# Optimization experiments

Hardware: AMD Instinct MI355X
Metric: run time of the kernel (lower is better)

Reference implementation:

```python
import jax, jax.numpy as jnp
import numpy as np
import math

DIM = 768
HEADS = 12
HEAD_DIM = DIM // HEADS
HIDDEN = DIM * 4
EPS = 1e-5

def _ln(x, g, b):
    mu = jnp.mean(x, axis=-1, keepdims=True)
    var = jnp.var(x, axis=-1, keepdims=True)
    return (x - mu) * jax.lax.rsqrt(var + EPS) * g + b

def setup_inputs() -> dict:
    key = jax.random.key(0)
    ks = jax.random.split(key, 16)
    def w(k, shape, fan_in):
        lim = 1.0 / math.sqrt(fan_in)
        return jax.random.uniform(k, shape, jnp.float32, -lim, lim)
    x = jax.random.normal(ks[0], (16, 1024, DIM), jnp.float32)
    return {
        "x": x,
        "ln1_g": jnp.ones((DIM,)), "ln1_b": jnp.zeros((DIM,)),
        "qkv_w": w(ks[1], (DIM, 3 * DIM), DIM), "qkv_b": w(ks[2], (3 * DIM,), DIM),
        "proj_w": w(ks[3], (DIM, DIM), DIM), "proj_b": w(ks[4], (DIM,), DIM),
        "ln2_g": jnp.ones((DIM,)), "ln2_b": jnp.zeros((DIM,)),
        "fc1_w": w(ks[5], (DIM, HIDDEN), DIM), "fc1_b": w(ks[6], (HIDDEN,), DIM),
        "fc2_w": w(ks[7], (HIDDEN, DIM), HIDDEN), "fc2_b": w(ks[8], (DIM,), HIDDEN),
        "ln3_g": jnp.ones((DIM,)), "ln3_b": jnp.zeros((DIM,)),
    }

def reference(x, ln1_g, ln1_b, qkv_w, qkv_b, proj_w, proj_b,
              ln2_g, ln2_b, fc1_w, fc1_b, fc2_w, fc2_b, ln3_g, ln3_b):
    B, N, _ = x.shape
    x_norm1 = _ln(x, ln1_g, ln1_b)
    qkv = x_norm1 @ qkv_w + qkv_b                      # [B,N,3*DIM]
    qkv = qkv.reshape(B, N, 3, HEADS, HEAD_DIM).transpose(2, 0, 3, 1, 4)
    q, k, v = qkv[0], qkv[1], qkv[2]                   # [B,H,N,Dh]
    scores = jnp.einsum('bhnd,bhmd->bhnm', q, k) / math.sqrt(HEAD_DIM)
    probs = jax.nn.softmax(scores, axis=-1)
    ctx = jnp.einsum('bhnm,bhmd->bhnd', probs, v)      # [B,H,N,Dh]
    ctx = ctx.transpose(0, 2, 1, 3).reshape(B, N, DIM)
    attn_out = ctx @ proj_w + proj_b
    x_after_attn = x + attn_out
    ff_in = _ln(x_after_attn, ln2_g, ln2_b)
    # NOTE: residual is taken from the NORMALIZED tensor, as in the source
    ff_hidden = jax.nn.gelu(ff_in @ fc1_w + fc1_b, approximate=False)
    ff_out = ff_hidden @ fc2_w + fc2_b
    x_after_mlp = ff_in + ff_out
    return _ln(x_after_mlp, ln3_g, ln3_b)
```

## Files before the change

kernel.cpp:

```cpp
#include <hip/hip_runtime.h>
#include <hip/hip_bf16.h>
#include <math.h>

#define NSEQ 1024
#define BB   16
#define DIM  768
#define NH   12
#define DH   64
#define HID  3072
#define QKVN 2304

typedef __hip_bfloat16 bf16;
typedef __attribute__((ext_vector_type(8))) short short8;
typedef __attribute__((ext_vector_type(4))) float floatx4;

__device__ __forceinline__ float b2f(bf16 v) { return __bfloat162float(v); }
__device__ __forceinline__ bf16 f2b(float v) { return __float2bfloat16(v); }
__device__ __forceinline__ unsigned short bbits(float v) {
    bf16 x = __float2bfloat16(v);
    return *reinterpret_cast<unsigned short*>(&x);
}
__device__ __forceinline__ float us2f(unsigned short u) {
    return b2f(*reinterpret_cast<bf16*>(&u));
}

__device__ __forceinline__ void gload16(const bf16* g, bf16* l) {
    __builtin_amdgcn_global_load_lds(
        (__attribute__((address_space(1))) void*)g,
        (__attribute__((address_space(3))) void*)l,
        16, 0, 0);
}

__device__ __forceinline__ bool mode_f32(const unsigned* sent) {
    return sent[0] == 0x3F800000u;
}
__device__ __forceinline__ float ldM(const void* p, long i, bool f32) {
    return f32 ? ((const float*)p)[i] : b2f(((const bf16*)p)[i]);
}

__global__ __launch_bounds__(256)
void ln_kernel(const void* __restrict__ in, long in_off, int in_ext,
               const void* __restrict__ g, const void* __restrict__ b,
               void* __restrict__ out, long out_off, int out_ext,
               const unsigned* __restrict__ sent) {
    bool m = mode_f32(sent);
    bool inF = in_ext && m, outF = out_ext && m;
    int wid = threadIdx.x >> 6, lane = threadIdx.x & 63;
    long row = (long)blockIdx.x * 4 + wid;
    float v[12];
    for (int j = 0; j < 3; ++j) {
        long idx = in_off + row * DIM + lane * 4 + j * 256;
        if (inF) {
            float4 t = *(const float4*)((const float*)in + idx);
            v[j * 4 + 0] = t.x; v[j * 4 + 1] = t.y;
            v[j * 4 + 2] = t.z; v[j * 4 + 3] = t.w;
        } else {
            ushort4 t = *(const ushort4*)((const bf16*)in + idx);
            v[j * 4 + 0] = us2f(t.x); v[j * 4 + 1] = us2f(t.y);
            v[j * 4 + 2] = us2f(t.z); v[j * 4 + 3] = us2f(t.w);
        }
    }
    float s = 0.f, q = 0.f;
    for (int i = 0; i < 12; ++i) { s += v[i]; q += v[i] * v[i]; }
    for (int off = 1; off < 64; off <<= 1) {
        s += __shfl_xor(s, off);
        q += __shfl_xor(q, off);
    }
    float mean = s * (1.0f / DIM);
    float var  = q * (1.0f / DIM) - mean * mean;
    float rs   = rsqrtf(var + 1e-5f);
    for (int j = 0; j < 3; ++j) {
        int col = lane * 4 + j * 256;
        float gv[4], bv[4];
        if (m) {
            float4 tg = *(const float4*)((const float*)g + col);
            float4 tb = *(const float4*)((const float*)b + col);
            gv[0] = tg.x; gv[1] = tg.y; gv[2] = tg.z; gv[3] = tg.w;
            bv[0] = tb.x; bv[1] = tb.y; bv[2] = tb.z; bv[3] = tb.w;
        } else {
            ushort4 tg = *(const ushort4*)((const bf16*)g + col);
            ushort4 tb = *(const ushort4*)((const bf16*)b + col);
            gv[0] = us2f(tg.x); gv[1] = us2f(tg.y); gv[2] = us2f(tg.z); gv[3] = us2f(tg.w);
            bv[0] = us2f(tb.x); bv[1] = us2f(tb.y); bv[2] = us2f(tb.z); bv[3] = us2f(tb.w);
        }
        float o[4];
        for (int k = 0; k < 4; ++k)
            o[k] = (v[j * 4 + k] - mean) * rs * gv[k] + bv[k];
        long idx = out_off + row * DIM + col;
        if (outF) {
            float4 t; t.x = o[0]; t.y = o[1]; t.z = o[2]; t.w = o[3];
            *(float4*)((float*)out + idx) = t;
        } else {
            ushort4 t;
            t.x = bbits(o[0]); t.y = bbits(o[1]); t.z = bbits(o[2]); t.w = bbits(o[3]);
            *(ushort4*)((bf16*)out + idx) = t;
        }
    }
}

__global__ __launch_bounds__(256)
void transpose_w(const void* __restrict__ W, bf16* __restrict__ WT,
                 int K, int N, const unsigned* __restrict__ sent) {
    bool m = mode_f32(sent);
    __shared__ float T[32][33];
    int t = threadIdx.x;
    int k0 = blockIdx.y * 32, n0 = blockIdx.x * 32;
    for (int i = 0; i < 4; ++i) {
        int r = (t >> 5) + i * 8, c = t & 31;
        T[r][c] = ldM(W, (long)(k0 + r) * N + n0 + c, m);
    }
    __syncthreads();
    for (int i = 0; i < 4; ++i) {
        int rr = (t >> 5) + i * 8, cc = t & 31;
        WT[(long)(n0 + rr) * K + k0 + cc] = f2b(T[cc][rr]);
    }
}

__global__ __launch_bounds__(256)
void v_transpose(const bf16* __restrict__ qkv, bf16* __restrict__ VT) {
    __shared__ bf16 T[32][33];
    int t = threadIdx.x;
    int c0 = blockIdx.x * 32, n0 = blockIdx.y * 32;
    const bf16* qb = qkv + (long)blockIdx.z * NSEQ * QKVN;
    bf16* vb = VT + (long)blockIdx.z * DIM * NSEQ;
    for (int i = 0; i < 4; ++i) {
        int r = (t >> 5) + i * 8, c = t & 31;
        T[r][c] = qb[(long)(n0 + r) * QKVN + 2 * DIM + c0 + c];
    }
    __syncthreads();
    for (int i = 0; i < 4; ++i) {
        int rr = (t >> 5) + i * 8, cc = t & 31;
        vb[(long)(c0 + rr) * NSEQ + n0 + cc] = T[cc][rr];
    }
}

__global__ __launch_bounds__(256)
void gemm_mfma(const bf16* __restrict__ A, const bf16* __restrict__ WT,
               const void* __restrict__ bias,
               const void* __restrict__ resid, long resid_off, int resid_ext,
               bf16* __restrict__ C, int M, int N, int K, int gelu_flag,
               const unsigned* __restrict__ sent) {
    __shared__ __align__(16) bf16 SH[2][128 * 64];
    bf16* As = SH[0];
    bf16* Bs = SH[1];
    int t = threadIdx.x;
    int wid = t >> 6, lane = t & 63;
    int quad = lane >> 4, l16 = lane & 15;
    int wm = (wid & 1) * 64, wn = (wid >> 1) * 64;
    int m0 = blockIdx.y * 128, n0 = blockIdx.x * 128;

    floatx4 acc[4][4];
    for (int i = 0; i < 4; ++i) for (int j = 0; j < 4; ++j)
        acc[i][j] = (floatx4){0.f, 0.f, 0.f, 0.f};

    int srow = lane >> 3;
    int sgc  = (lane & 7) ^ (srow & 7);

    for (int k0 = 0; k0 < K; k0 += 64) {
        #pragma unroll
        for (int j = 0; j < 4; ++j) {
            int br = (wid * 4 + j) * 8;
            gload16(&A[(long)(m0 + br + srow) * K + k0 + sgc * 8],
                    &As[br * 64]);
            gload16(&WT[(long)(n0 + br + srow) * K + k0 + sgc * 8],
                    &Bs[br * 64]);
        }
        __syncthreads();
        for (int ks = 0; ks < 2; ++ks) {
            int cq = ks * 4 + quad;
            short8 af[4], bfr[4];
            for (int mi = 0; mi < 4; ++mi)
                af[mi] = *(const short8*)(
                    &As[(wm + mi * 16 + l16) * 64 + ((cq ^ (l16 & 7)) << 3)]);
            for (int ni = 0; ni < 4; ++ni)
                bfr[ni] = *(const short8*)(
                    &Bs[(wn + ni * 16 + l16) * 64 + ((cq ^ (l16 & 7)) << 3)]);
            for (int mi = 0; mi < 4; ++mi)
                for (int ni = 0; ni < 4; ++ni)
                    acc[mi][ni] = __builtin_amdgcn_mfma_f32_16x16x32_bf16(
                        af[mi], bfr[ni], acc[mi][ni], 0, 0, 0);
        }
        __syncthreads();
    }

    bool md = mode_f32(sent);

    bf16* wreg = &SH[wid >> 1][(wid & 1) * (64 * 64)];
    for (int mi = 0; mi < 4; ++mi) {
        for (int ni = 0; ni < 4; ++ni) {
            int col = n0 + wn + ni * 16 + l16;
            float bv = ldM(bias, col, md);
            int chunk = ni * 2 + (l16 >> 3);
            int csw = chunk ^ (quad << 1);
            for (int r = 0; r < 4; ++r) {
                float v = acc[mi][ni][r] + bv;
                if (gelu_flag) v = 0.5f * v * (1.0f + erff(v * 0.70710678118f));
                int row_l = mi * 16 + quad * 4 + r;
                wreg[row_l * 64 + csw * 8 + (l16 & 7)] = f2b(v);
            }
        }
    }
    for (int s = 0; s < 8; ++s) {
        int row_l = s * 8 + (lane >> 3);
        int csw = (lane & 7) ^ (((row_l >> 2) & 3) << 1);
        short8 cv = *(const short8*)(&wreg[row_l * 64 + csw * 8]);
        long idx = (long)(m0 + wm + row_l) * N + n0 + wn + (lane & 7) * 8;
        if (resid) {
            float f[8];
            if (resid_ext && md) {
                const float* rp = (const float*)resid + resid_off + idx;
                float4 r0 = *(const float4*)(rp);
                float4 r1 = *(const float4*)(rp + 4);
                f[0] = r0.x; f[1] = r0.y; f[2] = r0.z; f[3] = r0.w;
                f[4] = r1.x; f[5] = r1.y; f[6] = r1.z; f[7] = r1.w;
            } else {
                const bf16* rp = resid_ext ? (const bf16*)resid + resid_off + idx
                                           : (const bf16*)resid + idx;
                short8 rv = *(const short8*)(rp);
                for (int j = 0; j < 8; ++j) {
                    short sj = rv[j];
                    f[j] = b2f(*reinterpret_cast<bf16*>(&sj));
                }
            }
            short8 ov;
            for (int j = 0; j < 8; ++j) {
                short sj = cv[j];
                float v = b2f(*reinterpret_cast<bf16*>(&sj)) + f[j];
                ov[j] = (short)bbits(v);
            }
            *(short8*)(&C[idx]) = ov;
        } else {
            *(short8*)(&C[idx]) = cv;
        }
    }
}

__global__ __launch_bounds__(256)
void attn_kernel(const bf16* __restrict__ qkv, const bf16* __restrict__ VT,
                 bf16* __restrict__ ctx) {
    const bf16* qb  = qkv + (long)blockIdx.z * NSEQ * QKVN;
    bf16*       cb  = ctx + (long)blockIdx.z * NSEQ * DIM;
    int h = blockIdx.y;
    const bf16* vtb = VT + ((long)blockIdx.z * DIM + h * DH) * NSEQ;
    int q0 = blockIdx.x * 64;
    int t = threadIdx.x;
    int wid = t >> 6, lane = t & 63;
    int quad = lane >> 4, l16 = lane & 15;

    __shared__ __align__(16) bf16 Qs[64 * 64];
    __shared__ __align__(16) bf16 Ks[64 * 64];
    __shared__ __align__(16) bf16 Vt[64 * 64];
    __shared__ bf16 Ps[4 * 16 * 72];

    int srow = t >> 2, cb2 = (t & 3) * 2;
    int sw0 = (cb2 ^ (srow & 7)) << 3;
    int sw1 = ((cb2 + 1) ^ (srow & 7)) << 3;

    {
        const bf16* src = qb + (long)(q0 + srow) * QKVN + h * DH + cb2 * 8;
        *(uint4*)(&Qs[srow * 64 + sw0]) = *(const uint4*)(src);
        *(uint4*)(&Qs[srow * 64 + sw1]) = *(const uint4*)(src + 8);
    }

    floatx4 Oc[4];
    for (int nt = 0; nt < 4; ++nt) Oc[nt] = (floatx4){0.f, 0.f, 0.f, 0.f};
    float mrow = -1e30f, lrow = 0.0f;

    bf16* Pw = &Ps[wid * 16 * 72];
    short8 af[2];
    bool afload = false;

    for (int kt = 0; kt < NSEQ / 64; ++kt) {
        __syncthreads();
        {
            const bf16* src = qb + (long)(kt * 64 + srow) * QKVN + DIM + h * DH + cb2 * 8;
            *(uint4*)(&Ks[srow * 64 + sw0]) = *(const uint4*)(src);
            *(uint4*)(&Ks[srow * 64 + sw1]) = *(const uint4*)(src + 8);
        }
        {
            const bf16* src = vtb + (long)srow * NSEQ + kt * 64 + cb2 * 8;
            *(uint4*)(&Vt[srow * 64 + sw0]) = *(const uint4*)(src);
            *(uint4*)(&Vt[srow * 64 + sw1]) = *(const uint4*)(src + 8);
        }
        __syncthreads();

        if (!afload) {
            for (int ks = 0; ks < 2; ++ks) {
                int cq = ks * 4 + quad;
                af[ks] = *(const short8*)(
                    &Qs[(wid * 16 + l16) * 64 + ((cq ^ (l16 & 7)) << 3)]);
            }
            afload = true;
        }

        floatx4 Sc[4];
        for (int kb = 0; kb < 4; ++kb) {
            floatx4 s = (floatx4){0.f, 0.f, 0.f, 0.f};
            for (int ks = 0; ks < 2; ++ks) {
                int cq = ks * 4 + quad;
                short8 kf = *(const short8*)(
                    &Ks[(kb * 16 + l16) * 64 + ((cq ^ (l16 & 7)) << 3)]);
                s = __builtin_amdgcn_mfma_f32_16x16x32_bf16(kf, af[ks], s, 0, 0, 0);
            }
            Sc[kb] = s;
        }

        float mx = -1e30f;
        for (int kb = 0; kb < 4; ++kb)
            for (int r = 0; r < 4; ++r)
                mx = fmaxf(mx, Sc[kb][r]);
        mx = fmaxf(mx, __shfl_xor(mx, 16));
        mx = fmaxf(mx, __shfl_xor(mx, 32));
        float smax = mx * 0.125f;
        if (!__all(smax <= mrow + 8.0f)) {
            float mnew = fmaxf(mrow, smax);
            float alpha = __expf(mrow - mnew);
            mrow = mnew;
            lrow *= alpha;
            float al[4];
            for (int r = 0; r < 4; ++r)
                al[r] = __shfl(alpha, quad * 4 + r);
            for (int nt = 0; nt < 4; ++nt)
                for (int r = 0; r < 4; ++r)
                    Oc[nt][r] *= al[r];
        }
        float su = 0.f;
        for (int kb = 0; kb < 4; ++kb)
            for (int r = 0; r < 4; ++r) {
                float p = __expf(Sc[kb][r] * 0.125f - mrow);
                Sc[kb][r] = p;
                su += p;
            }
        su += __shfl_xor(su, 16);
        su += __shfl_xor(su, 32);
        lrow += su;

        for (int kb = 0; kb < 4; ++kb)
            for (int r = 0; r < 4; ++r)
                Pw[l16 * 72 + kb * 16 + quad * 4 + r] = f2b(Sc[kb][r]);

        for (int ks = 0; ks < 2; ++ks) {
            int cq = ks * 4 + quad;
            short8 pf = *(const short8*)(&Pw[l16 * 72 + ks * 32 + quad * 8]);
            for (int nt = 0; nt < 4; ++nt) {
                short8 vf = *(const short8*)(
                    &Vt[(nt * 16 + l16) * 64 + ((cq ^ (l16 & 7)) << 3)]);
                Oc[nt] = __builtin_amdgcn_mfma_f32_16x16x32_bf16(pf, vf, Oc[nt], 0, 0, 0);
            }
        }
    }

    float inv[4];
    for (int r = 0; r < 4; ++r)
        inv[r] = 1.0f / __shfl(lrow, quad * 4 + r);
    for (int nt = 0; nt < 4; ++nt) {
        for (int r = 0; r < 4; ++r) {
            int q = q0 + wid * 16 + quad * 4 + r;
            cb[(long)q * DIM + h * DH + nt * 16 + l16] = f2b(Oc[nt][r] * inv[r]);
        }
    }
}

extern "C" void kernel_launch(void* const* d_in, const int* in_sizes, int n_in,
                              void* d_out, int out_size, void* d_ws, size_t ws_size,
                              hipStream_t stream) {
    const void* x      = d_in[0];
    const void* ln1_g  = d_in[1];
    const void* ln1_b  = d_in[2];
    const void* qkv_w  = d_in[3];
    const void* qkv_b  = d_in[4];
    const void* proj_w = d_in[5];
    const void* proj_b = d_in[6];
    const void* ln2_g  = d_in[7];
    const void* ln2_b  = d_in[8];
    const void* fc1_w  = d_in[9];
    const void* fc1_b  = d_in[10];
    const void* fc2_w  = d_in[11];
    const void* fc2_b  = d_in[12];
    const void* ln3_g  = d_in[13];
    const void* ln3_b  = d_in[14];
    const unsigned* sent = (const unsigned*)d_in[1];

    bf16* WTq = (bf16*)d_ws;
    bf16* WTp = WTq + (long)QKVN * DIM;
    bf16* WT1 = WTp + (long)DIM * DIM;
    bf16* WT2 = WT1 + (long)HID * DIM;
    bf16* A0  = WT2 + (long)DIM * HID;
    size_t wbytes = ((size_t)QKVN * DIM + (size_t)DIM * DIM +
                     (size_t)HID * DIM + (size_t)DIM * HID) * sizeof(bf16);

    int G = BB;
    while (G > 1 && wbytes + (size_t)G * NSEQ * 7680 > ws_size) G >>= 1;
    int TG = G * NSEQ;
    int CHT = (TG / 2 < 8192) ? TG / 2 : 8192;
    int nch = TG / CHT;

    bf16* W0 = A0;
    bf16* WQ = A0 + (long)TG * DIM;
    bf16* X2 = WQ;
    bf16* WH = WQ + (long)TG * DIM;
    bf16* VT = WQ + (long)TG * QKVN;

    transpose_w<<<dim3(QKVN / 32, DIM / 32), 256, 0, stream>>>(qkv_w, WTq, DIM, QKVN, sent);
    transpose_w<<<dim3(DIM / 32, DIM / 32), 256, 0, stream>>>(proj_w, WTp, DIM, DIM, sent);
    transpose_w<<<dim3(HID / 32, DIM / 32), 256, 0, stream>>>(fc1_w, WT1, DIM, HID, sent);
    transpose_w<<<dim3(DIM / 32, HID / 32), 256, 0, stream>>>(fc2_w, WT2, HID, DIM, sent);

    for (int g = 0; g < BB / G; ++g) {
        long xoff = (long)g * TG * DIM;

        ln_kernel<<<TG / 4, 256, 0, stream>>>(x, xoff, 1, ln1_g, ln1_b, W0, 0, 0, sent);
        gemm_mfma<<<dim3(QKVN / 128, TG / 128), 256, 0, stream>>>(
            W0, WTq, qkv_b, nullptr, 0, 0, WQ, TG, QKVN, DIM, 0, sent);
        v_transpose<<<dim3(DIM / 32, NSEQ / 32, G), 256, 0, stream>>>(WQ, VT);
        attn_kernel<<<dim3(NSEQ / 64, NH, G), 256, 0, stream>>>(WQ, VT, W0);
        gemm_mfma<<<dim3(DIM / 128, TG / 128), 256, 0, stream>>>(
            W0, WTp, proj_b, x, xoff, 1, X2, TG, DIM, DIM, 0, sent);
        ln_kernel<<<TG / 4, 256, 0, stream>>>(X2, 0, 0, ln2_g, ln2_b, X2, 0, 0, sent);
        for (int c = 0; c < nch; ++c) {
            bf16* ffc = X2 + (long)c * CHT * DIM;
            gemm_mfma<<<dim3(HID / 128, CHT / 128), 256, 0, stream>>>(
                ffc, WT1, fc1_b, nullptr, 0, 0, WH, CHT, HID, DIM, 1, sent);
            gemm_mfma<<<dim3(DIM / 128, CHT / 128), 256, 0, stream>>>(
                WH, WT2, fc2_b, ffc, 0, 0, W0 + (long)c * CHT * DIM,
                CHT, DIM, HID, 0, sent);
        }
        ln_kernel<<<TG / 4, 256, 0, stream>>>(W0, 0, 0, ln3_g, ln3_b, d_out, xoff, 1, sent);
    }
}
```

Before: 715.4 us.

## Add 256x256-tile 512-thread MFMA GEMM for QKV and FC1 projections

Introduces a new GEMM kernel with 256x256 output tiles, 8 waves, a 4-stage LDS ring buffer with two tiles of prefetch in flight, swizzled LDS layout, and an LDS-staged epilogue for coalesced stores. It replaces the 128x128 GEMM for the QKV and FC1 projections to raise arithmetic intensity and data reuse per block. The trade-off is more LDS and register use per block and fewer blocks in the grid, which may reduce occupancy and wave-level load balance across CUs.

```diff
diff --git a/kernel.cpp b/kernel.cpp
--- a/kernel.cpp
+++ b/kernel.cpp
@@ -235,6 +235,106 @@
     }
 }
 
+__device__ __forceinline__ void stg256(const bf16* src, long row0, int K, int k0,
+                                       bf16* lds, int wid, int lane, int sgc) {
+    gload16(&src[(row0 + wid * 16 + (lane >> 2)) * (long)K + k0 + sgc * 8],
+            &lds[wid * 16 * 32]);
+}
+
+__global__ __launch_bounds__(512)
+void gemm_mfma256(const bf16* __restrict__ A, const bf16* __restrict__ WT,
+                  const void* __restrict__ bias, bf16* __restrict__ C,
+                  int M, int N, int K, int gelu_flag,
+                  const unsigned* __restrict__ sent) {
+    __shared__ __align__(16) bf16 SH[4][2][256 * 32];
+    int t = threadIdx.x;
+    int wid = t >> 6, lane = t & 63;
+    int quad = lane >> 4, l16 = lane & 15;
+    int wm = (wid >> 2) * 128, wn = (wid & 3) * 64;
+    long m0 = (long)blockIdx.y * 256, n0 = (long)blockIdx.x * 256;
+    int sgc = (lane & 3) ^ ((lane >> 2) & 3);
+    int rsw = (quad ^ (l16 & 3)) << 3;
+
+    floatx4 acc[8][4];
+    #pragma unroll
+    for (int i = 0; i < 8; ++i)
+        #pragma unroll
+        for (int j = 0; j < 4; ++j)
+            acc[i][j] = (floatx4){0.f, 0.f, 0.f, 0.f};
+
+    int NT = K >> 5;
+    for (int tt = 0; tt < 2; ++tt) {
+        int k0 = tt * 32;
+        stg256(A,  m0,       K, k0, SH[tt][0],            wid, lane, sgc);
+        stg256(A,  m0 + 128, K, k0, SH[tt][0] + 128 * 32, wid, lane, sgc);
+        stg256(WT, n0,       K, k0, SH[tt][1],            wid, lane, sgc);
+        stg256(WT, n0 + 128, K, k0, SH[tt][1] + 128 * 32, wid, lane, sgc);
+    }
+    asm volatile("s_waitcnt vmcnt(4)" ::: "memory");
+    __builtin_amdgcn_s_barrier();
+
+    for (int kt = 0; kt < NT; ++kt) {
+        bf16* Ab = SH[kt & 3][0];
+        bf16* Bb = SH[kt & 3][1];
+        bool pre = (kt + 2 < NT);
+        int b2 = (kt + 2) & 3;
+        int k2 = (kt + 2) * 32;
+
+        short8 bfr[4];
+        #pragma unroll
+        for (int ni = 0; ni < 4; ++ni)
+            bfr[ni] = *(const short8*)(&Bb[(wn + ni * 16 + l16) * 32 + rsw]);
+
+        #pragma unroll
+        for (int p = 0; p < 4; ++p) {
+            if (pre) {
+                if (p == 0) stg256(A,  m0,       K, k2, SH[b2][0],            wid, lane, sgc);
+                if (p == 1) stg256(A,  m0 + 128, K, k2, SH[b2][0] + 128 * 32, wid, lane, sgc);
+                if (p == 2) stg256(WT, n0,       K, k2, SH[b2][1],            wid, lane, sgc);
+                if (p == 3) stg256(WT, n0 + 128, K, k2, SH[b2][1] + 128 * 32, wid, lane, sgc);
+            }
+            short8 af0 = *(const short8*)(&Ab[(wm + (p * 2)     * 16 + l16) * 32 + rsw]);
+            short8 af1 = *(const short8*)(&Ab[(wm + (p * 2 + 1) * 16 + l16) * 32 + rsw]);
+            __builtin_amdgcn_s_setprio(1);
+            #pragma unroll
+            for (int ni = 0; ni < 4; ++ni) {
+                acc[p * 2][ni] = __builtin_amdgcn_mfma_f32_16x16x32_bf16(
+                    af0, bfr[ni], acc[p * 2][ni], 0, 0, 0);
+                acc[p * 2 + 1][ni] = __builtin_amdgcn_mfma_f32_16x16x32_bf16(
+                    af1, bfr[ni], acc[p * 2 + 1][ni], 0, 0, 0);
+            }
+            __builtin_amdgcn_s_setprio(0);
+        }
+        if (pre) asm volatile("s_waitcnt vmcnt(4)" ::: "memory");
+        else     asm volatile("s_waitcnt vmcnt(0)" ::: "memory");
+        __builtin_amdgcn_s_barrier();
+    }
+
+    bool md = mode_f32(sent);
+    bf16* wreg = &SH[0][0][0] + wid * 8192;
+    for (int mi = 0; mi < 8; ++mi) {
+        for (int ni = 0; ni < 4; ++ni) {
+            long col = n0 + wn + ni * 16 + l16;
+            float bv = ldM(bias, col, md);
+            int chunk = ni * 2 + (l16 >> 3);
+            int csw = chunk ^ (quad << 1);
+            for (int r = 0; r < 4; ++r) {
+                float v = acc[mi][ni][r] + bv;
+                if (gelu_flag) v = 0.5f * v * (1.0f + erff(v * 0.70710678118f));
+                int row_l = mi * 16 + quad * 4 + r;
+                wreg[row_l * 64 + csw * 8 + (l16 & 7)] = f2b(v);
+            }
+        }
+    }
+    for (int s = 0; s < 16; ++s) {
+        int row_l = s * 8 + (lane >> 3);
+        int csw = (lane & 7) ^ (((row_l >> 2) & 3) << 1);
+        short8 cv = *(const short8*)(&wreg[row_l * 64 + csw * 8]);
+        long idx = (m0 + wm + row_l) * N + n0 + wn + (lane & 7) * 8;
+        *(short8*)(&C[idx]) = cv;
+    }
+}
+
 __global__ __launch_bounds__(256)
 void attn_kernel(const bf16* __restrict__ qkv, const bf16* __restrict__ VT,
                  bf16* __restrict__ ctx) {
@@ -410,8 +510,8 @@
         long xoff = (long)g * TG * DIM;
 
         ln_kernel<<<TG / 4, 256, 0, stream>>>(x, xoff, 1, ln1_g, ln1_b, W0, 0, 0, sent);
-        gemm_mfma<<<dim3(QKVN / 128, TG / 128), 256, 0, stream>>>(
-            W0, WTq, qkv_b, nullptr, 0, 0, WQ, TG, QKVN, DIM, 0, sent);
+        gemm_mfma256<<<dim3(QKVN / 256, TG / 256), 512, 0, stream>>>(
+            W0, WTq, qkv_b, WQ, TG, QKVN, DIM, 0, sent);
         v_transpose<<<dim3(DIM / 32, NSEQ / 32, G), 256, 0, stream>>>(WQ, VT);
         attn_kernel<<<dim3(NSEQ / 64, NH, G), 256, 0, stream>>>(WQ, VT, W0);
         gemm_mfma<<<dim3(DIM / 128, TG / 128), 256, 0, stream>>>(
@@ -419,8 +519,8 @@
         ln_kernel<<<TG / 4, 256, 0, stream>>>(X2, 0, 0, ln2_g, ln2_b, X2, 0, 0, sent);
         for (int c = 0; c < nch; ++c) {
             bf16* ffc = X2 + (long)c * CHT * DIM;
-            gemm_mfma<<<dim3(HID / 128, CHT / 128), 256, 0, stream>>>(
-                ffc, WT1, fc1_b, nullptr, 0, 0, WH, CHT, HID, DIM, 1, sent);
+            gemm_mfma256<<<dim3(HID / 256, CHT / 256), 512, 0, stream>>>(
+                ffc, WT1, fc1_b, WH, CHT, HID, DIM, 1, sent);
             gemm_mfma<<<dim3(DIM / 128, CHT / 128), 256, 0, stream>>>(
                 WH, WT2, fc2_b, ffc, 0, 0, W0 + (long)c * CHT * DIM,
                 CHT, DIM, HID, 0, sent);
```

After: 748.5 us. 1.05x slower.
